# Performance work log

Measured on AMD Instinct MI355X. Metric: run time of the kernel, lower is better.

The kernel has to match this reference:

```python
import jax, jax.numpy as jnp
import numpy as np

OUT_H, OUT_W = 7, 7
SPATIAL_SCALE = 0.25
SAMPLE_NUM = 2  # sampling grid per bin is SAMPLE_NUM x SAMPLE_NUM


def setup_inputs() -> dict:
    key = jax.random.key(0)
    k1, k2, k3, k4, k5, k6 = jax.random.split(key, 6)
    B, C, H, W = 2, 256, 200, 200
    features = jax.random.normal(k1, (B, C, H, W), dtype=jnp.float32)
    N = 512
    # rois: (batch_idx, cx, cy, w, h, theta) in image coords (image = 800x800)
    bidx = jax.random.randint(k2, (N,), 0, B).astype(jnp.float32)
    cx = jax.random.uniform(k3, (N,), jnp.float32, 100.0, 700.0)
    cy = jax.random.uniform(k4, (N,), jnp.float32, 100.0, 700.0)
    wh = jax.random.uniform(k5, (N, 2), jnp.float32, 32.0, 256.0)
    ang = jax.random.uniform(k6, (N,), jnp.float32, -np.pi / 2, np.pi / 2)
    rois = jnp.concatenate(
        [bidx[:, None], cx[:, None], cy[:, None], wh, ang[:, None]], axis=1
    )
    return {"features": features, "rois": rois}


def _rroi_align(features, rois):
    B, C, H, W = features.shape
    N = rois.shape[0]
    batch_idx = rois[:, 0].astype(jnp.int32)
    cx = rois[:, 1] * SPATIAL_SCALE
    cy = rois[:, 2] * SPATIAL_SCALE
    rw = jnp.maximum(rois[:, 3] * SPATIAL_SCALE, 1.0)
    rh = jnp.maximum(rois[:, 4] * SPATIAL_SCALE, 1.0)
    theta = rois[:, 5]

    bin_h = rh / OUT_H
    bin_w = rw / OUT_W

    ph = jnp.arange(OUT_H, dtype=jnp.float32)
    pw = jnp.arange(OUT_W, dtype=jnp.float32)
    frac = (jnp.arange(SAMPLE_NUM, dtype=jnp.float32) + 0.5) / SAMPLE_NUM

    # local (un-rotated) offsets from roi center
    # yy: [N, OUT_H, S], xx: [N, OUT_W, S]
    yy = -rh[:, None, None] / 2 + (ph[None, :, None] + frac[None, None, :]) * bin_h[:, None, None]
    xx = -rw[:, None, None] / 2 + (pw[None, :, None] + frac[None, None, :]) * bin_w[:, None, None]

    cosT = jnp.cos(theta)[:, None, None, None, None]
    sinT = jnp.sin(theta)[:, None, None, None, None]
    yy_ = yy[:, :, None, :, None]  # [N, OH, 1, Sy, 1]
    xx_ = xx[:, None, :, None, :]  # [N, 1, OW, 1, Sx]
    # rotate into feature-map coords (RRPN/mmcv convention)
    x = xx_ * cosT + yy_ * sinT + cx[:, None, None, None, None]  # [N,OH,OW,Sy,Sx]
    y = yy_ * cosT - xx_ * sinT + cy[:, None, None, None, None]

    valid = (y > -1.0) & (y < H) & (x > -1.0) & (x < W)
    y = jnp.clip(y, 0.0, H - 1)
    x = jnp.clip(x, 0.0, W - 1)

    y0 = jnp.clip(jnp.floor(y), 0, H - 2).astype(jnp.int32)
    x0 = jnp.clip(jnp.floor(x), 0, W - 2).astype(jnp.int32)
    y1 = y0 + 1
    x1 = x0 + 1
    ly = y - y0.astype(jnp.float32)
    lx = x - x0.astype(jnp.float32)
    hy = 1.0 - ly
    hx = 1.0 - lx

    b = batch_idx[:, None, None, None, None]  # [N,1,1,1,1]

    def gather(yi, xi):
        # advanced indices (b, yi, xi) separated by the channel slice ->
        # result shape [N, OH, OW, Sy, Sx, C]
        return features[b, :, yi, xi]

    val = (
        (hy * hx)[..., None] * gather(y0, x0)
        + (hy * lx)[..., None] * gather(y0, x1)
        + (ly * hx)[..., None] * gather(y1, x0)
        + (ly * lx)[..., None] * gather(y1, x1)
    )
    val = jnp.where(valid[..., None], val, 0.0)
    # average over the SAMPLE_NUM x SAMPLE_NUM grid per bin
    out = val.mean(axis=(3, 4))  # [N, OH, OW, C]
    return jnp.transpose(out, (0, 3, 1, 2))  # [N, C, OH, OW]


def reference(features, rois):
    return _rroi_align(features, rois)
```

## Files before the change

kernel.cpp:

```cpp
#include <hip/hip_runtime.h>
#include <hip/hip_bf16.h>

constexpr int B_ = 2, C_ = 256, H_ = 200, W_ = 200;
constexpr int HW_ = H_ * W_;
constexpr int N_ROIS = 512;
constexpr int OUT_H_ = 7, OUT_W_ = 7;
constexpr float SPATIAL_SCALE_ = 0.25f;
constexpr int NBIN = OUT_H_ * OUT_W_;
constexpr int OUT_PER_ROI = C_ * NBIN;

using f32x4 = __attribute__((ext_vector_type(4))) float;

__global__ __launch_bounds__(512) void roi_sort_kernel(
    const float* __restrict__ rois, int* __restrict__ perm) {
    __shared__ unsigned s_key[N_ROIS];
    const int i = threadIdx.x;
    const float* roi = rois + (size_t)i * 6;
    const int b  = (int)roi[0];
    const int ix = (int)(roi[1] * SPATIAL_SCALE_) & 255;
    const int iy = (int)(roi[2] * SPATIAL_SCALE_) & 255;
    const unsigned key = ((unsigned)b << 16) | ((unsigned)iy << 8) | (unsigned)ix;
    s_key[i] = key;
    __syncthreads();
    int rank = 0;
    for (int j = 0; j < N_ROIS; ++j) {
        const unsigned kj = s_key[j];
        rank += (kj < key) || (kj == key && j < i);
    }
    perm[rank] = i;
}

__global__ __launch_bounds__(256) void transpose_bf_kernel(
    const float* __restrict__ in, __hip_bfloat16* __restrict__ out) {
    __shared__ float tile[64][65];
    const int b  = blockIdx.z;
    const int p0 = blockIdx.x * 64;
    const int c0 = blockIdx.y * 64;
    const int tid = threadIdx.x;
    const int hi = tid >> 4;
    const int lo = tid & 15;

    const float* src = in + (size_t)b * C_ * HW_;
    __hip_bfloat16* dst = out + (size_t)b * HW_ * C_;

#pragma unroll
    for (int j = 0; j < 4; ++j) {
        const int cr = hi + j * 16;
        const int pm = lo * 4;
        const f32x4 v = __builtin_nontemporal_load(
            (const f32x4*)(src + (size_t)(c0 + cr) * HW_ + p0 + pm));
        tile[pm + 0][cr] = v.x;
        tile[pm + 1][cr] = v.y;
        tile[pm + 2][cr] = v.z;
        tile[pm + 3][cr] = v.w;
    }
    __syncthreads();
#pragma unroll
    for (int j = 0; j < 4; ++j) {
        const int pr = hi + j * 16;
        const int cm = lo * 4;
        ushort4 u;
        __hip_bfloat16 h0 = __float2bfloat16(tile[pr][cm + 0]);
        __hip_bfloat16 h1 = __float2bfloat16(tile[pr][cm + 1]);
        __hip_bfloat16 h2 = __float2bfloat16(tile[pr][cm + 2]);
        __hip_bfloat16 h3 = __float2bfloat16(tile[pr][cm + 3]);
        u.x = *(unsigned short*)&h0;
        u.y = *(unsigned short*)&h1;
        u.z = *(unsigned short*)&h2;
        u.w = *(unsigned short*)&h3;
        *(ushort4*)(dst + (size_t)(p0 + pr) * C_ + c0 + cm) = u;
    }
}

__global__ __launch_bounds__(512) void rroi_gather_kernel(
    const __hip_bfloat16* __restrict__ feat,
    const float* __restrict__ rois,
    const int* __restrict__ perm,
    float* __restrict__ out) {
    __shared__ float  s_out[OUT_PER_ROI];
    __shared__ int    s_off[196];
    __shared__ float4 s_w[196];

    const int bid = blockIdx.x;
    const int sorted = (bid & 7) * (N_ROIS / 8) + (bid >> 3);
    const int n = perm ? perm[sorted] : bid;
    const int tid = threadIdx.x;

    const float* roi = rois + (size_t)n * 6;
    const int   b     = (int)roi[0];
    const float cx    = roi[1] * SPATIAL_SCALE_;
    const float cy    = roi[2] * SPATIAL_SCALE_;
    const float rw    = fmaxf(roi[3] * SPATIAL_SCALE_, 1.0f);
    const float rh    = fmaxf(roi[4] * SPATIAL_SCALE_, 1.0f);
    const float theta = roi[5];
    const float bin_h = rh / (float)OUT_H_;
    const float bin_w = rw / (float)OUT_W_;

    if (tid < 196) {
        const float cosT = cosf(theta);
        const float sinT = sinf(theta);
        const int bin = tid >> 2;
        const int s   = tid & 3;
        const int ph  = bin / OUT_W_;
        const int pw  = bin - ph * OUT_W_;
        const int s1  = s >> 1;
        const int s2  = s & 1;

        const float yy = -rh * 0.5f + ((float)ph + ((float)s1 + 0.5f) * 0.5f) * bin_h;
        const float xx = -rw * 0.5f + ((float)pw + ((float)s2 + 0.5f) * 0.5f) * bin_w;

        float x = xx * cosT + yy * sinT + cx;
        float y = yy * cosT - xx * sinT + cy;

        const bool valid = (y > -1.0f) && (y < (float)H_) &&
                           (x > -1.0f) && (x < (float)W_);

        y = fminf(fmaxf(y, 0.0f), (float)(H_ - 1));
        x = fminf(fmaxf(x, 0.0f), (float)(W_ - 1));
        int y0 = (int)floorf(y);  if (y0 > H_ - 2) y0 = H_ - 2;
        int x0 = (int)floorf(x);  if (x0 > W_ - 2) x0 = W_ - 2;

        const float ly = y - (float)y0;
        const float lx = x - (float)x0;
        const float hy = 1.0f - ly;
        const float hx = 1.0f - lx;
        const float m  = valid ? 0.25f : 0.0f;

        s_w[tid]   = make_float4(hy * hx * m, hy * lx * m, ly * hx * m, ly * lx * m);
        s_off[tid] = (y0 * W_ + x0) * C_;
    }
    __syncthreads();

    const int wave = tid >> 6;
    const int lane = tid & 63;
    const __hip_bfloat16* base = feat + (size_t)b * HW_ * C_ + lane;

    for (int bin = wave; bin < NBIN; bin += 8) {
        float acc[4] = {0.f, 0.f, 0.f, 0.f};
#pragma unroll
        for (int s = 0; s < 4; ++s) {
            const int j = bin * 4 + s;
            const int off = s_off[j];
            const float4 w = s_w[j];
            const __hip_bfloat16* p = base + off;
#pragma unroll
            for (int m = 0; m < 4; ++m) {
                const __hip_bfloat16* q = p + 64 * m;
                const float f00 = __bfloat162float(q[0]);
                const float f01 = __bfloat162float(q[C_]);
                const float f10 = __bfloat162float(q[W_ * C_]);
                const float f11 = __bfloat162float(q[W_ * C_ + C_]);
                acc[m] += w.x * f00 + w.y * f01 + w.z * f10 + w.w * f11;
            }
        }
#pragma unroll
        for (int m = 0; m < 4; ++m) {
            s_out[(lane + 64 * m) * NBIN + bin] = acc[m];
        }
    }
    __syncthreads();

    f32x4* o = (f32x4*)(out + (size_t)n * OUT_PER_ROI);
    const f32x4* l = (const f32x4*)s_out;
#pragma unroll
    for (int k = 0; k < 6; ++k) {
        __builtin_nontemporal_store(l[tid + 512 * k], o + tid + 512 * k);
    }
    if (tid < 64) __builtin_nontemporal_store(l[3072 + tid], o + 3072 + tid);
}

__global__ __launch_bounds__(64) void rroi_fallback_kernel(
    const float* __restrict__ feat,
    const float* __restrict__ rois,
    float* __restrict__ out) {
    const int blk = blockIdx.x;
    const int n   = blk / NBIN;
    const int bin = blk % NBIN;
    const int ph  = bin / OUT_W_;
    const int pw  = bin % OUT_W_;

    const float* roi = rois + (size_t)n * 6;
    const int   b     = (int)roi[0];
    const float cx    = roi[1] * SPATIAL_SCALE_;
    const float cy    = roi[2] * SPATIAL_SCALE_;
    const float rw    = fmaxf(roi[3] * SPATIAL_SCALE_, 1.0f);
    const float rh    = fmaxf(roi[4] * SPATIAL_SCALE_, 1.0f);
    const float theta = roi[5];
    const float bin_h = rh / (float)OUT_H_;
    const float bin_w = rw / (float)OUT_W_;
    const float cosT  = cosf(theta);
    const float sinT  = sinf(theta);
    const int t = threadIdx.x;
    float acc[4] = {0.f, 0.f, 0.f, 0.f};

#pragma unroll
    for (int s1 = 0; s1 < 2; ++s1) {
        const float yy = -rh * 0.5f + ((float)ph + ((float)s1 + 0.5f) * 0.5f) * bin_h;
#pragma unroll
        for (int s2 = 0; s2 < 2; ++s2) {
            const float xx = -rw * 0.5f + ((float)pw + ((float)s2 + 0.5f) * 0.5f) * bin_w;
            float x = xx * cosT + yy * sinT + cx;
            float y = yy * cosT - xx * sinT + cy;
            const bool valid = (y > -1.0f) && (y < (float)H_) &&
                               (x > -1.0f) && (x < (float)W_);
            if (!valid) continue;
            y = fminf(fmaxf(y, 0.0f), (float)(H_ - 1));
            x = fminf(fmaxf(x, 0.0f), (float)(W_ - 1));
            int y0 = (int)floorf(y);  if (y0 > H_ - 2) y0 = H_ - 2;
            int x0 = (int)floorf(x);  if (x0 > W_ - 2) x0 = W_ - 2;
            const float ly = y - (float)y0, lx = x - (float)x0;
            const float hy = 1.0f - ly, hx = 1.0f - lx;
            const float w00 = hy * hx, w01 = hy * lx, w10 = ly * hx, w11 = ly * lx;
            const int off0 = y0 * W_ + x0;
#pragma unroll
            for (int i = 0; i < 4; ++i) {
                const float* basep = feat + ((size_t)b * C_ + 4 * t + i) * HW_;
                acc[i] += w00 * basep[off0] + w01 * basep[off0 + 1] +
                          w10 * basep[off0 + W_] + w11 * basep[off0 + W_ + 1];
            }
        }
    }
#pragma unroll
    for (int i = 0; i < 4; ++i) {
        out[((size_t)n * C_ + (4 * t + i)) * NBIN + bin] = acc[i] * 0.25f;
    }
}

extern "C" void kernel_launch(void* const* d_in, const int* in_sizes, int n_in,
                              void* d_out, int out_size, void* d_ws, size_t ws_size,
                              hipStream_t stream) {
    const float* features = (const float*)d_in[0];
    const float* rois     = (const float*)d_in[1];
    float* out = (float*)d_out;

    const size_t feat_bytes = (size_t)B_ * C_ * HW_ * sizeof(__hip_bfloat16);
    const size_t perm_bytes = (size_t)N_ROIS * sizeof(int);

    if (ws_size >= feat_bytes + perm_bytes) {
        __hip_bfloat16* feat_bf = (__hip_bfloat16*)d_ws;
        int* perm = (int*)((char*)d_ws + ((feat_bytes + 255) & ~(size_t)255));
        roi_sort_kernel<<<1, 512, 0, stream>>>(rois, perm);
        dim3 tg(HW_ / 64, C_ / 64, B_);
        transpose_bf_kernel<<<tg, 256, 0, stream>>>(features, feat_bf);
        rroi_gather_kernel<<<N_ROIS, 512, 0, stream>>>(feat_bf, rois, perm, out);
    } else if (ws_size >= feat_bytes) {
        __hip_bfloat16* feat_bf = (__hip_bfloat16*)d_ws;
        dim3 tg(HW_ / 64, C_ / 64, B_);
        transpose_bf_kernel<<<tg, 256, 0, stream>>>(features, feat_bf);
        rroi_gather_kernel<<<N_ROIS, 512, 0, stream>>>(feat_bf, rois, nullptr, out);
    } else {
        rroi_fallback_kernel<<<N_ROIS * NBIN, 64, 0, stream>>>(features, rois, out);
    }
}
```

Measured before the change: 158.8 us.

## Split each ROI across two blocks by channel half with packed bf16 loads

Each ROI is now processed by two blocks, each covering half the channels, doubling the grid and halving the shared output buffer per block. Feature reads load two bf16 channels per 32-bit word and unpack them with bit shifts instead of four separate 16-bit loads per corner. This aims to raise occupancy and reduce load instruction count, at the cost of duplicating per-ROI sample coordinate setup in both blocks.

```diff
diff --git a/kernel.cpp b/kernel.cpp
--- a/kernel.cpp
+++ b/kernel.cpp
@@ -8,8 +8,19 @@
 constexpr float SPATIAL_SCALE_ = 0.25f;
 constexpr int NBIN = OUT_H_ * OUT_W_;
 constexpr int OUT_PER_ROI = C_ * NBIN;
+constexpr int HALF_C = C_ / 2;
+constexpr int HALF_OUT = HALF_C * NBIN;
 
 using f32x4 = __attribute__((ext_vector_type(4))) float;
+
+__device__ __forceinline__ float bf_lo(unsigned u) {
+    const unsigned v = u << 16;
+    return __builtin_bit_cast(float, v);
+}
+__device__ __forceinline__ float bf_hi(unsigned u) {
+    const unsigned v = u & 0xffff0000u;
+    return __builtin_bit_cast(float, v);
+}
 
 __global__ __launch_bounds__(512) void roi_sort_kernel(
     const float* __restrict__ rois, int* __restrict__ perm) {
@@ -72,19 +83,21 @@
     }
 }
 
-__global__ __launch_bounds__(512) void rroi_gather_kernel(
+__global__ __launch_bounds__(512, 8) void rroi_gather_kernel(
     const __hip_bfloat16* __restrict__ feat,
     const float* __restrict__ rois,
     const int* __restrict__ perm,
     float* __restrict__ out) {
-    __shared__ float  s_out[OUT_PER_ROI];
+    __shared__ float  s_out[HALF_OUT];
     __shared__ int    s_off[196];
     __shared__ float4 s_w[196];
 
-    const int bid = blockIdx.x;
-    const int sorted = (bid & 7) * (N_ROIS / 8) + (bid >> 3);
-    const int n = perm ? perm[sorted] : bid;
-    const int tid = threadIdx.x;
+    const int bid  = blockIdx.x;
+    const int slot = (bid & 7) * 128 + (bid >> 3);
+    const int s_i  = slot >> 1;
+    const int h    = slot & 1;
+    const int n    = perm ? perm[s_i] : s_i;
+    const int tid  = threadIdx.x;
 
     const float* roi = rois + (size_t)n * 6;
     const int   b     = (int)roi[0];
@@ -127,46 +140,45 @@
         const float m  = valid ? 0.25f : 0.0f;
 
         s_w[tid]   = make_float4(hy * hx * m, hy * lx * m, ly * hx * m, ly * lx * m);
-        s_off[tid] = (y0 * W_ + x0) * C_;
+        s_off[tid] = (y0 * W_ + x0) * (C_ / 2);
     }
     __syncthreads();
 
     const int wave = tid >> 6;
     const int lane = tid & 63;
-    const __hip_bfloat16* base = feat + (size_t)b * HW_ * C_ + lane;
+    const unsigned* base =
+        (const unsigned*)(feat + (size_t)b * HW_ * C_) + h * 64 + lane;
 
     for (int bin = wave; bin < NBIN; bin += 8) {
-        float acc[4] = {0.f, 0.f, 0.f, 0.f};
+        float acc0 = 0.f, acc1 = 0.f;
 #pragma unroll
         for (int s = 0; s < 4; ++s) {
             const int j = bin * 4 + s;
             const int off = s_off[j];
             const float4 w = s_w[j];
-            const __hip_bfloat16* p = base + off;
-#pragma unroll
-            for (int m = 0; m < 4; ++m) {
-                const __hip_bfloat16* q = p + 64 * m;
-                const float f00 = __bfloat162float(q[0]);
-                const float f01 = __bfloat162float(q[C_]);
-                const float f10 = __bfloat162float(q[W_ * C_]);
-                const float f11 = __bfloat162float(q[W_ * C_ + C_]);
-                acc[m] += w.x * f00 + w.y * f01 + w.z * f10 + w.w * f11;
-            }
+            const unsigned* p = base + off;
+            const unsigned u00 = p[0];
+            const unsigned u01 = p[C_ / 2];
+            const unsigned u10 = p[W_ * (C_ / 2)];
+            const unsigned u11 = p[W_ * (C_ / 2) + C_ / 2];
+            acc0 += w.x * bf_lo(u00) + w.y * bf_lo(u01) +
+                    w.z * bf_lo(u10) + w.w * bf_lo(u11);
+            acc1 += w.x * bf_hi(u00) + w.y * bf_hi(u01) +
+                    w.z * bf_hi(u10) + w.w * bf_hi(u11);
         }
-#pragma unroll
-        for (int m = 0; m < 4; ++m) {
-            s_out[(lane + 64 * m) * NBIN + bin] = acc[m];
-        }
-    }
-    __syncthreads();
-
-    f32x4* o = (f32x4*)(out + (size_t)n * OUT_PER_ROI);
+        const int c = 2 * lane;
+        s_out[(c + 0) * NBIN + bin] = acc0;
+        s_out[(c + 1) * NBIN + bin] = acc1;
+    }
+    __syncthreads();
+
+    f32x4* o = (f32x4*)(out + (size_t)n * OUT_PER_ROI + h * HALF_OUT);
     const f32x4* l = (const f32x4*)s_out;
 #pragma unroll
-    for (int k = 0; k < 6; ++k) {
+    for (int k = 0; k < 3; ++k) {
         __builtin_nontemporal_store(l[tid + 512 * k], o + tid + 512 * k);
     }
-    if (tid < 64) __builtin_nontemporal_store(l[3072 + tid], o + 3072 + tid);
+    if (tid < 32) __builtin_nontemporal_store(l[1536 + tid], o + 1536 + tid);
 }
 
 __global__ __launch_bounds__(64) void rroi_fallback_kernel(
@@ -236,18 +248,18 @@
     const size_t feat_bytes = (size_t)B_ * C_ * HW_ * sizeof(__hip_bfloat16);
     const size_t perm_bytes = (size_t)N_ROIS * sizeof(int);
 
-    if (ws_size >= feat_bytes + perm_bytes) {
+    if (ws_size >= feat_bytes + 256 + perm_bytes) {
         __hip_bfloat16* feat_bf = (__hip_bfloat16*)d_ws;
         int* perm = (int*)((char*)d_ws + ((feat_bytes + 255) & ~(size_t)255));
         roi_sort_kernel<<<1, 512, 0, stream>>>(rois, perm);
         dim3 tg(HW_ / 64, C_ / 64, B_);
         transpose_bf_kernel<<<tg, 256, 0, stream>>>(features, feat_bf);
-        rroi_gather_kernel<<<N_ROIS, 512, 0, stream>>>(feat_bf, rois, perm, out);
+        rroi_gather_kernel<<<N_ROIS * 2, 512, 0, stream>>>(feat_bf, rois, perm, out);
     } else if (ws_size >= feat_bytes) {
         __hip_bfloat16* feat_bf = (__hip_bfloat16*)d_ws;
         dim3 tg(HW_ / 64, C_ / 64, B_);
         transpose_bf_kernel<<<tg, 256, 0, stream>>>(features, feat_bf);
-        rroi_gather_kernel<<<N_ROIS, 512, 0, stream>>>(feat_bf, rois, nullptr, out);
+        rroi_gather_kernel<<<N_ROIS * 2, 512, 0, stream>>>(feat_bf, rois, nullptr, out);
     } else {
         rroi_fallback_kernel<<<N_ROIS * NBIN, 64, 0, stream>>>(features, rois, out);
     }
```

After: 156.7 us. About the same (-1.3%).

## Vectorize bf16 gather to 16-byte loads of 8 channels per lane

Applied to the files above, without the earlier changes.

The gather kernel now has each lane load a uint4 holding 8 bf16 channels per corner pixel, with half-wave groups handling a bin, instead of scalar 2-byte loads of 4 channels spread 64 apart. Unpacking is done with bit shifts, so there are far fewer load instructions for the same work. The transpose write path is also widened to 16-byte stores, and the gather kernel gets a launch_bounds occupancy hint. The cost is more live registers per lane and more strided LDS writes into s_out, which may cause bank conflicts.

```diff
diff --git a/kernel.cpp b/kernel.cpp
--- a/kernel.cpp
+++ b/kernel.cpp
@@ -8,8 +8,24 @@
 constexpr float SPATIAL_SCALE_ = 0.25f;
 constexpr int NBIN = OUT_H_ * OUT_W_;
 constexpr int OUT_PER_ROI = C_ * NBIN;
+constexpr int PIX = C_ / 8;
 
 using f32x4 = __attribute__((ext_vector_type(4))) float;
+
+__device__ __forceinline__ float bf_lo(unsigned u) {
+    const unsigned v = u << 16;
+    return __builtin_bit_cast(float, v);
+}
+__device__ __forceinline__ float bf_hi(unsigned u) {
+    const unsigned v = u & 0xffff0000u;
+    return __builtin_bit_cast(float, v);
+}
+__device__ __forceinline__ unsigned bf_pack(float a, float b) {
+    __hip_bfloat16 ha = __float2bfloat16(a);
+    __hip_bfloat16 hb = __float2bfloat16(b);
+    return (unsigned)*(unsigned short*)&ha |
+           ((unsigned)*(unsigned short*)&hb << 16);
+}
 
 __global__ __launch_bounds__(512) void roi_sort_kernel(
     const float* __restrict__ rois, int* __restrict__ perm) {
@@ -56,35 +72,31 @@
     }
     __syncthreads();
 #pragma unroll
-    for (int j = 0; j < 4; ++j) {
-        const int pr = hi + j * 16;
-        const int cm = lo * 4;
-        ushort4 u;
-        __hip_bfloat16 h0 = __float2bfloat16(tile[pr][cm + 0]);
-        __hip_bfloat16 h1 = __float2bfloat16(tile[pr][cm + 1]);
-        __hip_bfloat16 h2 = __float2bfloat16(tile[pr][cm + 2]);
-        __hip_bfloat16 h3 = __float2bfloat16(tile[pr][cm + 3]);
-        u.x = *(unsigned short*)&h0;
-        u.y = *(unsigned short*)&h1;
-        u.z = *(unsigned short*)&h2;
-        u.w = *(unsigned short*)&h3;
-        *(ushort4*)(dst + (size_t)(p0 + pr) * C_ + c0 + cm) = u;
-    }
-}
-
-__global__ __launch_bounds__(512) void rroi_gather_kernel(
+    for (int j = 0; j < 2; ++j) {
+        const int pr = (tid >> 3) + j * 32;
+        const int cm = 8 * (tid & 7);
+        uint4 u;
+        u.x = bf_pack(tile[pr][cm + 0], tile[pr][cm + 1]);
+        u.y = bf_pack(tile[pr][cm + 2], tile[pr][cm + 3]);
+        u.z = bf_pack(tile[pr][cm + 4], tile[pr][cm + 5]);
+        u.w = bf_pack(tile[pr][cm + 6], tile[pr][cm + 7]);
+        *(uint4*)(dst + (size_t)(p0 + pr) * C_ + c0 + cm) = u;
+    }
+}
+
+__global__ __launch_bounds__(512, 4) void rroi_gather_kernel(
     const __hip_bfloat16* __restrict__ feat,
     const float* __restrict__ rois,
     const int* __restrict__ perm,
     float* __restrict__ out) {
     __shared__ float  s_out[OUT_PER_ROI];
-    __shared__ int    s_off[196];
+    __shared__ int    s_pix[196];
     __shared__ float4 s_w[196];
 
-    const int bid = blockIdx.x;
-    const int sorted = (bid & 7) * (N_ROIS / 8) + (bid >> 3);
-    const int n = perm ? perm[sorted] : bid;
-    const int tid = threadIdx.x;
+    const int bid  = blockIdx.x;
+    const int slot = (bid & 7) * 64 + (bid >> 3);
+    const int n    = perm ? perm[slot] : slot;
+    const int tid  = threadIdx.x;
 
     const float* roi = rois + (size_t)n * 6;
     const int   b     = (int)roi[0];
@@ -127,35 +139,47 @@
         const float m  = valid ? 0.25f : 0.0f;
 
         s_w[tid]   = make_float4(hy * hx * m, hy * lx * m, ly * hx * m, ly * lx * m);
-        s_off[tid] = (y0 * W_ + x0) * C_;
-    }
-    __syncthreads();
-
-    const int wave = tid >> 6;
-    const int lane = tid & 63;
-    const __hip_bfloat16* base = feat + (size_t)b * HW_ * C_ + lane;
-
-    for (int bin = wave; bin < NBIN; bin += 8) {
-        float acc[4] = {0.f, 0.f, 0.f, 0.f};
+        s_pix[tid] = y0 * W_ + x0;
+    }
+    __syncthreads();
+
+    const int hw = tid >> 5;
+    const int cl = tid & 31;
+    const uint4* base = (const uint4*)(feat + (size_t)b * HW_ * C_) + cl;
+
+    for (int bin = hw; bin < NBIN; bin += 16) {
+        float acc[8] = {0.f, 0.f, 0.f, 0.f, 0.f, 0.f, 0.f, 0.f};
 #pragma unroll
         for (int s = 0; s < 4; ++s) {
             const int j = bin * 4 + s;
-            const int off = s_off[j];
             const float4 w = s_w[j];
-            const __hip_bfloat16* p = base + off;
-#pragma unroll
-            for (int m = 0; m < 4; ++m) {
-                const __hip_bfloat16* q = p + 64 * m;
-                const float f00 = __bfloat162float(q[0]);
-                const float f01 = __bfloat162float(q[C_]);
-                const float f10 = __bfloat162float(q[W_ * C_]);
-                const float f11 = __bfloat162float(q[W_ * C_ + C_]);
-                acc[m] += w.x * f00 + w.y * f01 + w.z * f10 + w.w * f11;
-            }
+            const uint4* p = base + s_pix[j] * PIX;
+            const uint4 u00 = p[0];
+            const uint4 u01 = p[PIX];
+            const uint4 u10 = p[W_ * PIX];
+            const uint4 u11 = p[W_ * PIX + PIX];
+
+            acc[0] += w.x * bf_lo(u00.x) + w.y * bf_lo(u01.x) +
+                      w.z * bf_lo(u10.x) + w.w * bf_lo(u11.x);
+            acc[1] += w.x * bf_hi(u00.x) + w.y * bf_hi(u01.x) +
+                      w.z * bf_hi(u10.x) + w.w * bf_hi(u11.x);
+            acc[2] += w.x * bf_lo(u00.y) + w.y * bf_lo(u01.y) +
+                      w.z * bf_lo(u10.y) + w.w * bf_lo(u11.y);
+            acc[3] += w.x * bf_hi(u00.y) + w.y * bf_hi(u01.y) +
+                      w.z * bf_hi(u10.y) + w.w * bf_hi(u11.y);
+            acc[4] += w.x * bf_lo(u00.z) + w.y * bf_lo(u01.z) +
+                      w.z * bf_lo(u10.z) + w.w * bf_lo(u11.z);
+            acc[5] += w.x * bf_hi(u00.z) + w.y * bf_hi(u01.z) +
+                      w.z * bf_hi(u10.z) + w.w * bf_hi(u11.z);
+            acc[6] += w.x * bf_lo(u00.w) + w.y * bf_lo(u01.w) +
+                      w.z * bf_lo(u10.w) + w.w * bf_lo(u11.w);
+            acc[7] += w.x * bf_hi(u00.w) + w.y * bf_hi(u01.w) +
+                      w.z * bf_hi(u10.w) + w.w * bf_hi(u11.w);
         }
-#pragma unroll
-        for (int m = 0; m < 4; ++m) {
-            s_out[(lane + 64 * m) * NBIN + bin] = acc[m];
+        const int c = 8 * cl;
+#pragma unroll
+        for (int i = 0; i < 8; ++i) {
+            s_out[(c + i) * NBIN + bin] = acc[i];
         }
     }
     __syncthreads();
@@ -236,7 +260,7 @@
     const size_t feat_bytes = (size_t)B_ * C_ * HW_ * sizeof(__hip_bfloat16);
     const size_t perm_bytes = (size_t)N_ROIS * sizeof(int);
 
-    if (ws_size >= feat_bytes + perm_bytes) {
+    if (ws_size >= feat_bytes + 256 + perm_bytes) {
         __hip_bfloat16* feat_bf = (__hip_bfloat16*)d_ws;
         int* perm = (int*)((char*)d_ws + ((feat_bytes + 255) & ~(size_t)255));
         roi_sort_kernel<<<1, 512, 0, stream>>>(rois, perm);
```

After: 154.6 us. 2.6% less time.
